# Performance work log

Hardware: AMD Instinct MI355X
Metric: run time of the kernel (lower is better)

## Reference

```python
import jax, jax.numpy as jnp
import numpy as np

LB = 8      # luma bins
CM = 1      # channel multiplier
GC = 16     # guide complexity
NIN, NOUT = 4, 3
BN_EPS = 1e-5


def bilateral_slice(grid, guide):
    # grid: [B, gh, gw, gd, C]; guide: [B, H, W] in [0,1]
    B, gh, gw, gd, C = grid.shape
    _, H, W = guide.shape
    dt = guide.dtype
    hg = (jnp.arange(H, dtype=dt) + 0.5) * (gh / H) - 0.5   # [H]
    wg = (jnp.arange(W, dtype=dt) + 0.5) * (gw / W) - 0.5   # [W]
    zg = guide * gd - 0.5                                    # [B,H,W]
    h0 = jnp.floor(hg); w0 = jnp.floor(wg); z0 = jnp.floor(zg)
    fh = hg - h0; fw = wg - w0; fz = zg - z0
    h0 = h0.astype(jnp.int32); w0 = w0.astype(jnp.int32); z0 = z0.astype(jnp.int32)
    bidx = jnp.arange(B)[:, None, None]
    out = jnp.zeros((B, H, W, C), dtype=grid.dtype)
    for dh in (0, 1):
        hi = jnp.clip(h0 + dh, 0, gh - 1)          # [H]
        wh_h = fh if dh else (1.0 - fh)
        for dw in (0, 1):
            wi = jnp.clip(w0 + dw, 0, gw - 1)      # [W]
            wh_w = fw if dw else (1.0 - fw)
            w_hw = (wh_h[:, None] * wh_w[None, :])[None]  # [1,H,W]
            for dz in (0, 1):
                zi = jnp.clip(z0 + dz, 0, gd - 1)  # [B,H,W]
                wh_z = fz if dz else (1.0 - fz)
                g = grid[bidx, hi[None, :, None], wi[None, None, :], zi]  # [B,H,W,C]
                out = out + g * (w_hw * wh_z)[..., None]
    return out


def conv1x1(x, w, b):
    # x: [B,Cin,H,W], w: [Cout,Cin], b: [Cout]
    return jnp.einsum('oc,bchw->bohw', w, x) + b[None, :, None, None]


def setup_inputs() -> dict:
    key = jax.random.key(0)
    ks = jax.random.split(key, 12)
    B, H, W, GH, GW = 4, 1024, 1024, 16, 16
    fullres = jax.random.uniform(ks[0], (B, 3, H, W), dtype=jnp.float32)
    local_features = jax.random.normal(ks[1], (B, 8 * CM * LB, GH, GW), dtype=jnp.float32)
    global_features = jax.random.normal(ks[2], (B, 8 * CM * LB), dtype=jnp.float32)
    cout = LB * NOUT * NIN  # 96
    fusion_w = jax.random.normal(ks[3], (cout, 8 * CM * LB), dtype=jnp.float32) * 0.1
    fusion_b = jnp.zeros((cout,), dtype=jnp.float32)
    g1_w = jax.random.normal(ks[4], (GC, 3), dtype=jnp.float32) * 0.5
    g1_b = jnp.zeros((GC,), dtype=jnp.float32)
    bn_gamma = jnp.ones((GC,), dtype=jnp.float32)
    bn_beta = jnp.zeros((GC,), dtype=jnp.float32)
    bn_mean = jnp.zeros((GC,), dtype=jnp.float32)
    bn_var = jnp.ones((GC,), dtype=jnp.float32)
    g2_w = jax.random.normal(ks[5], (1, GC), dtype=jnp.float32) * 0.3
    g2_b = jnp.zeros((1,), dtype=jnp.float32)
    return dict(fullres=fullres, local_features=local_features, global_features=global_features,
                fusion_w=fusion_w, fusion_b=fusion_b, g1_w=g1_w, g1_b=g1_b,
                bn_gamma=bn_gamma, bn_beta=bn_beta, bn_mean=bn_mean, bn_var=bn_var,
                g2_w=g2_w, g2_b=g2_b)


def reference(fullres, local_features, global_features, fusion_w, fusion_b,
              g1_w, g1_b, bn_gamma, bn_beta, bn_mean, bn_var, g2_w, g2_b):
    B = fullres.shape[0]
    # Fusion: relu(local + broadcast global), then 1x1 conv to 96 channels
    fused = jax.nn.relu(local_features + global_features[:, :, None, None])
    x = conv1x1(fused, fusion_w, fusion_b)                    # [B,96,GH,GW]
    GH, GW = x.shape[2], x.shape[3]
    # split(12, dim=1) + stack(dim=2) -> [B,12,LB,GH,GW]
    coeffs = x.reshape(B, LB, NIN * NOUT, GH, GW).transpose(0, 2, 1, 3, 4)
    # GuideNN: 1x1 conv + BN(eval) + relu, then 1x1 conv + sigmoid
    g = conv1x1(fullres, g1_w, g1_b)
    g = (g - bn_mean[None, :, None, None]) * (bn_gamma[None, :, None, None] *
        jax.lax.rsqrt(bn_var + BN_EPS)[None, :, None, None]) + bn_beta[None, :, None, None]
    g = jax.nn.relu(g)
    guide = jax.nn.sigmoid(conv1x1(g, g2_w, g2_b))[:, 0]      # [B,H,W]
    # Slicing: permute grid to [B,GH,GW,LB,12], trilinear slice, back to NCHW
    grid = coeffs.transpose(0, 3, 4, 2, 1)
    sliced = bilateral_slice(grid, guide)                     # [B,H,W,12]
    coeff = sliced.transpose(0, 3, 1, 2)                      # [B,12,H,W]
    # ApplyCoeffs
    R = jnp.sum(fullres * coeff[:, 0:3], axis=1, keepdims=True) + coeff[:, 9:10]
    G = jnp.sum(fullres * coeff[:, 3:6], axis=1, keepdims=True) + coeff[:, 10:11]
    Bc = jnp.sum(fullres * coeff[:, 6:9], axis=1, keepdims=True) + coeff[:, 11:12]
    return jnp.tanh(jnp.concatenate([R, G, Bc], axis=1))
```

## Files before the change

### kernel.cpp

```cpp
#include <hip/hip_runtime.h>
#include <math.h>


#define GRIDBUF_FLOATS (4 * 16 * 16 * 96)
#define CELL_STRIDE 100

typedef float  vfloat4 __attribute__((ext_vector_type(4)));
typedef float  f2      __attribute__((ext_vector_type(2)));
typedef int    i2      __attribute__((ext_vector_type(2)));

__device__ inline f2 splat2(float x) { f2 v; v.x = x; v.y = x; return v; }

__device__ inline f2 fast_tanh2(f2 x) {
    f2 ax = __builtin_elementwise_abs(x);
    f2 xx = ax + ax;
    f2 e;
    e.x = __expf(xx.x);
    e.y = __expf(xx.y);
    f2 ep1 = e + splat2(1.0f);
    f2 r;
    r.x = __builtin_amdgcn_rcpf(ep1.x);
    r.y = __builtin_amdgcn_rcpf(ep1.y);
    f2 t = splat2(1.0f) - (r + r);
    i2 sgn = __builtin_bit_cast(i2, x) & (i2){(int)0x80000000, (int)0x80000000};
    return __builtin_bit_cast(f2, __builtin_bit_cast(i2, t) | sgn);
}

__global__ __launch_bounds__(128) void coeff_kernel(
    const float* __restrict__ lf,
    const float* __restrict__ gf,
    const float* __restrict__ fw,
    const float* __restrict__ fb,
    const float* __restrict__ g1w,
    const float* __restrict__ g1b,
    const float* __restrict__ bng,
    const float* __restrict__ bnb,
    const float* __restrict__ bnm,
    const float* __restrict__ bnv,
    const float* __restrict__ g2w,
    const float* __restrict__ g2b,
    float* __restrict__ gridbuf,
    float* __restrict__ params)
{
    __shared__ float fused[64];
    const int blk = blockIdx.x;
    const int b   = blk >> 8;
    const int pos = blk & 255;
    const int t   = threadIdx.x;

    if (t < 64) {
        float v = lf[(b * 64 + t) * 256 + pos] + gf[b * 64 + t];
        fused[t] = v > 0.0f ? v : 0.0f;
    }
    __syncthreads();

    if (t < 96) {
        float acc = fb[t];
        const float* wrow = fw + t * 64;
#pragma unroll
        for (int i = 0; i < 64; ++i) acc = fmaf(wrow[i], fused[i], acc);
        gridbuf[blk * 96 + t] = acc;
    }

    if (blk == 0 && t >= 96 && t < 112) {
        int k = t - 96;
        float a = bng[k] * rsqrtf(bnv[k] + 1e-5f);
        params[k]      = g1w[k * 3 + 0] * a;
        params[16 + k] = g1w[k * 3 + 1] * a;
        params[32 + k] = g1w[k * 3 + 2] * a;
        params[48 + k] = (g1b[k] - bnm[k]) * a + bnb[k];
        params[64 + k] = g2w[k];
        if (k == 0) params[80] = g2b[0];
    }
}

__global__ __launch_bounds__(256) void slice_apply_kernel(
    const float* __restrict__ fullres,
    const float* __restrict__ gridbuf,
    const float* __restrict__ params,
    float* __restrict__ out)
{
    __shared__ __align__(16) float hrow[16 * CELL_STRIDE];

    const int t    = threadIdx.x;
    const int blk  = blockIdx.x;
    const int b    = blk >> 11;
    const int rem  = blk & 2047;
    const int y    = rem >> 1;
    const int half = rem & 1;
    const int x0   = half << 9;

    const int xb      = x0 + (t << 1);
    const int pixbase = (y << 10) + xb;
    const int planeB  = (b * 3) << 20;

    f2 rr = *(const f2*)(fullres + planeB + (0 << 20) + pixbase);
    f2 gg = *(const f2*)(fullres + planeB + (1 << 20) + pixbase);
    f2 bb = *(const f2*)(fullres + planeB + (2 << 20) + pixbase);

    {
        const int h0i  = (y < 32) ? -1 : ((y - 32) >> 6);
        const float fh = ((float)y * 0.015625f + (0.0078125f - 0.5f)) - (float)h0i;
        const int hc0  = h0i < 0 ? 0 : h0i;
        const int hc1  = (h0i + 1) > 15 ? 15 : (h0i + 1);
        const float* row0 = gridbuf + (b * 256 + hc0 * 16) * 96;
        const float* row1 = gridbuf + (b * 256 + hc1 * 16) * 96;
        const float wfh0 = 1.0f - fh;
        const int cbase = half * 7;
        if (t < 216) {
            const int i   = cbase * 96 + (t << 2);
            const int wc  = i / 96;
            const int rm  = i - wc * 96;
            float4 a = *(const float4*)(row0 + i);
            float4 c = *(const float4*)(row1 + i);
            float4 r;
            r.x = fmaf(wfh0, a.x, fh * c.x);
            r.y = fmaf(wfh0, a.y, fh * c.y);
            r.z = fmaf(wfh0, a.z, fh * c.z);
            r.w = fmaf(wfh0, a.w, fh * c.w);
            *(float4*)(hrow + wc * CELL_STRIDE + rm) = r;
        }
    }
    __syncthreads();

    const int w0i = (xb < 32) ? -1 : ((xb - 32) >> 6);
    const int wc0 = w0i < 0 ? 0 : w0i;
    const int wc1 = (w0i + 1) > 15 ? 15 : (w0i + 1);
    const float fw0 = (float)xb * 0.015625f + (0.0078125f - 0.5f) - (float)w0i;
    const float* cell0 = hrow + wc0 * CELL_STRIDE;
    const float* cell1 = hrow + wc1 * CELL_STRIDE;

    f2 acc = splat2(params[80]);
#pragma unroll
    for (int k = 0; k < 16; ++k) {
        f2 gk = __builtin_elementwise_fma(rr, splat2(params[k]),
                __builtin_elementwise_fma(gg, splat2(params[16 + k]),
                __builtin_elementwise_fma(bb, splat2(params[32 + k]),
                                          splat2(params[48 + k]))));
        gk = __builtin_elementwise_max(gk, splat2(0.0f));
        acc = __builtin_elementwise_fma(gk, splat2(params[64 + k]), acc);
    }
    f2 zg;
    zg.x = fmaf(8.0f, __builtin_amdgcn_rcpf(1.0f + __expf(-acc.x)), -0.5f);
    zg.y = fmaf(8.0f, __builtin_amdgcn_rcpf(1.0f + __expf(-acc.y)), -0.5f);

    f2 Rp, Gp, Bp;
#pragma unroll
    for (int px = 0; px < 2; ++px) {
        const float zgp = px ? zg.y : zg.x;
        int   z0 = (int)floorf(zgp);
        float fz = zgp - (float)z0;
        int zc0 = z0 < 0 ? 0 : z0;
        int zc1 = (z0 + 1) > 7 ? 7 : (z0 + 1);

        const float fw_ = fw0 + (float)px * 0.015625f;
        const float ww0 = 1.0f - fw_;
        const f2 W00 = splat2(ww0 * (1.0f - fz));
        const f2 W01 = splat2(ww0 * fz);
        const f2 W10 = splat2(fw_ * (1.0f - fz));
        const f2 W11 = splat2(fw_ * fz);

        const float4* p00 = (const float4*)(cell0 + zc0 * 12);
        const float4* p01 = (const float4*)(cell0 + zc1 * 12);
        const float4* p10 = (const float4*)(cell1 + zc0 * 12);
        const float4* p11 = (const float4*)(cell1 + zc1 * 12);

        f2 sa[6];
#pragma unroll
        for (int q = 0; q < 3; ++q) {
            float4 a = p00[q], c = p01[q], d = p10[q], e = p11[q];
            f2 alo = (f2){a.x, a.y}, ahi = (f2){a.z, a.w};
            f2 clo = (f2){c.x, c.y}, chi = (f2){c.z, c.w};
            f2 dlo = (f2){d.x, d.y}, dhi = (f2){d.z, d.w};
            f2 elo = (f2){e.x, e.y}, ehi = (f2){e.z, e.w};
            sa[2 * q] =
                __builtin_elementwise_fma(alo, W00,
                __builtin_elementwise_fma(clo, W01,
                __builtin_elementwise_fma(dlo, W10, elo * W11)));
            sa[2 * q + 1] =
                __builtin_elementwise_fma(ahi, W00,
                __builtin_elementwise_fma(chi, W01,
                __builtin_elementwise_fma(dhi, W10, ehi * W11)));
        }

        const float rs = px ? rr.y : rr.x;
        const float gs = px ? gg.y : gg.x;
        const float bs = px ? bb.y : bb.x;
        float Rv = fmaf(rs, sa[0].x, fmaf(gs, sa[0].y, fmaf(bs, sa[1].x, sa[4].y)));
        float Gv = fmaf(rs, sa[1].y, fmaf(gs, sa[2].x, fmaf(bs, sa[2].y, sa[5].x)));
        float Bv = fmaf(rs, sa[3].x, fmaf(gs, sa[3].y, fmaf(bs, sa[4].x, sa[5].y)));
        if (px == 0) { Rp.x = Rv; Gp.x = Gv; Bp.x = Bv; }
        else         { Rp.y = Rv; Gp.y = Gv; Bp.y = Bv; }
    }

    f2 tR = fast_tanh2(Rp);
    f2 tG = fast_tanh2(Gp);
    f2 tB = fast_tanh2(Bp);

    __builtin_nontemporal_store(tR, (f2*)(out + planeB + (0 << 20) + pixbase));
    __builtin_nontemporal_store(tG, (f2*)(out + planeB + (1 << 20) + pixbase));
    __builtin_nontemporal_store(tB, (f2*)(out + planeB + (2 << 20) + pixbase));
}

extern "C" void kernel_launch(void* const* d_in, const int* in_sizes, int n_in,
                              void* d_out, int out_size, void* d_ws, size_t ws_size,
                              hipStream_t stream) {
    const float* fullres = (const float*)d_in[0];
    const float* lf      = (const float*)d_in[1];
    const float* gf      = (const float*)d_in[2];
    const float* fw      = (const float*)d_in[3];
    const float* fb      = (const float*)d_in[4];
    const float* g1w     = (const float*)d_in[5];
    const float* g1b     = (const float*)d_in[6];
    const float* bng     = (const float*)d_in[7];
    const float* bnb     = (const float*)d_in[8];
    const float* bnm     = (const float*)d_in[9];
    const float* bnv     = (const float*)d_in[10];
    const float* g2w     = (const float*)d_in[11];
    const float* g2b     = (const float*)d_in[12];
    float* out = (float*)d_out;

    float* gridbuf = (float*)d_ws;
    float* params  = gridbuf + GRIDBUF_FLOATS;

    coeff_kernel<<<4 * 256, 128, 0, stream>>>(lf, gf, fw, fb, g1w, g1b,
                                              bng, bnb, bnm, bnv, g2w, g2b,
                                              gridbuf, params);
    slice_apply_kernel<<<4 * 2048, 256, 0, stream>>>(fullres, gridbuf, params, out);
}
```

Before: 129.9 us.

## Loop over batch inside slice kernel with double-buffered LDS and prefetch

Each block now handles one row-half for all four batch images instead of one. It double-buffers the shared grid row and prefetches the next image's pixels and grid rows while computing the current one. This amortizes per-block setup (index math, coordinate computation) and overlaps global loads with compute. In exchange there are 4x fewer blocks (2048), which lowers occupancy and parallelism, and register pressure rises from the prefetched values.

```diff
diff --git a/kernel.cpp b/kernel.cpp
--- a/kernel.cpp
+++ b/kernel.cpp
@@ -5,9 +5,8 @@
 #define GRIDBUF_FLOATS (4 * 16 * 16 * 96)
 #define CELL_STRIDE 100
 
-typedef float  vfloat4 __attribute__((ext_vector_type(4)));
-typedef float  f2      __attribute__((ext_vector_type(2)));
-typedef int    i2      __attribute__((ext_vector_type(2)));
+typedef float  f2  __attribute__((ext_vector_type(2)));
+typedef int    i2  __attribute__((ext_vector_type(2)));
 
 __device__ inline f2 splat2(float x) { f2 v; v.x = x; v.y = x; return v; }
 
@@ -80,126 +79,147 @@
     const float* __restrict__ params,
     float* __restrict__ out)
 {
-    __shared__ __align__(16) float hrow[16 * CELL_STRIDE];
+    __shared__ __align__(16) float hbuf[2][16 * CELL_STRIDE];
 
     const int t    = threadIdx.x;
-    const int blk  = blockIdx.x;
-    const int b    = blk >> 11;
-    const int rem  = blk & 2047;
-    const int y    = rem >> 1;
-    const int half = rem & 1;
-    const int x0   = half << 9;
-
-    const int xb      = x0 + (t << 1);
+    const int i    = blockIdx.x;
+    const int y    = i >> 1;
+    const int half = i & 1;
+    const int xb   = (half << 9) + (t << 1);
     const int pixbase = (y << 10) + xb;
-    const int planeB  = (b * 3) << 20;
-
-    f2 rr = *(const f2*)(fullres + planeB + (0 << 20) + pixbase);
-    f2 gg = *(const f2*)(fullres + planeB + (1 << 20) + pixbase);
-    f2 bb = *(const f2*)(fullres + planeB + (2 << 20) + pixbase);
-
-    {
-        const int h0i  = (y < 32) ? -1 : ((y - 32) >> 6);
-        const float fh = ((float)y * 0.015625f + (0.0078125f - 0.5f)) - (float)h0i;
-        const int hc0  = h0i < 0 ? 0 : h0i;
-        const int hc1  = (h0i + 1) > 15 ? 15 : (h0i + 1);
-        const float* row0 = gridbuf + (b * 256 + hc0 * 16) * 96;
-        const float* row1 = gridbuf + (b * 256 + hc1 * 16) * 96;
-        const float wfh0 = 1.0f - fh;
-        const int cbase = half * 7;
-        if (t < 216) {
-            const int i   = cbase * 96 + (t << 2);
-            const int wc  = i / 96;
-            const int rm  = i - wc * 96;
-            float4 a = *(const float4*)(row0 + i);
-            float4 c = *(const float4*)(row1 + i);
-            float4 r;
-            r.x = fmaf(wfh0, a.x, fh * c.x);
-            r.y = fmaf(wfh0, a.y, fh * c.y);
-            r.z = fmaf(wfh0, a.z, fh * c.z);
-            r.w = fmaf(wfh0, a.w, fh * c.w);
-            *(float4*)(hrow + wc * CELL_STRIDE + rm) = r;
-        }
-    }
-    __syncthreads();
+
+    const int h0i  = (y < 32) ? -1 : ((y - 32) >> 6);
+    const float fh = ((float)y * 0.015625f + (0.0078125f - 0.5f)) - (float)h0i;
+    const int hc0  = h0i < 0 ? 0 : h0i;
+    const int hc1  = (h0i + 1) > 15 ? 15 : (h0i + 1);
+    const float wfh0 = 1.0f - fh;
+
+    const int cbase = half * 7;
+    const int fi   = cbase * 96 + (t << 2);
+    const int fwc  = fi / 96;
+    const int frm  = fi - fwc * 96;
+    const int fill_off = fwc * CELL_STRIDE + frm;
+    const float* grow0 = gridbuf + hc0 * 16 * 96 + fi;
+    const float* grow1 = gridbuf + hc1 * 16 * 96 + fi;
 
     const int w0i = (xb < 32) ? -1 : ((xb - 32) >> 6);
     const int wc0 = w0i < 0 ? 0 : w0i;
     const int wc1 = (w0i + 1) > 15 ? 15 : (w0i + 1);
     const float fw0 = (float)xb * 0.015625f + (0.0078125f - 0.5f) - (float)w0i;
-    const float* cell0 = hrow + wc0 * CELL_STRIDE;
-    const float* cell1 = hrow + wc1 * CELL_STRIDE;
-
-    f2 acc = splat2(params[80]);
-#pragma unroll
-    for (int k = 0; k < 16; ++k) {
-        f2 gk = __builtin_elementwise_fma(rr, splat2(params[k]),
-                __builtin_elementwise_fma(gg, splat2(params[16 + k]),
-                __builtin_elementwise_fma(bb, splat2(params[32 + k]),
-                                          splat2(params[48 + k]))));
-        gk = __builtin_elementwise_max(gk, splat2(0.0f));
-        acc = __builtin_elementwise_fma(gk, splat2(params[64 + k]), acc);
-    }
-    f2 zg;
-    zg.x = fmaf(8.0f, __builtin_amdgcn_rcpf(1.0f + __expf(-acc.x)), -0.5f);
-    zg.y = fmaf(8.0f, __builtin_amdgcn_rcpf(1.0f + __expf(-acc.y)), -0.5f);
-
-    f2 Rp, Gp, Bp;
-#pragma unroll
-    for (int px = 0; px < 2; ++px) {
-        const float zgp = px ? zg.y : zg.x;
-        int   z0 = (int)floorf(zgp);
-        float fz = zgp - (float)z0;
-        int zc0 = z0 < 0 ? 0 : z0;
-        int zc1 = (z0 + 1) > 7 ? 7 : (z0 + 1);
-
-        const float fw_ = fw0 + (float)px * 0.015625f;
-        const float ww0 = 1.0f - fw_;
-        const f2 W00 = splat2(ww0 * (1.0f - fz));
-        const f2 W01 = splat2(ww0 * fz);
-        const f2 W10 = splat2(fw_ * (1.0f - fz));
-        const f2 W11 = splat2(fw_ * fz);
-
-        const float4* p00 = (const float4*)(cell0 + zc0 * 12);
-        const float4* p01 = (const float4*)(cell0 + zc1 * 12);
-        const float4* p10 = (const float4*)(cell1 + zc0 * 12);
-        const float4* p11 = (const float4*)(cell1 + zc1 * 12);
-
-        f2 sa[6];
-#pragma unroll
-        for (int q = 0; q < 3; ++q) {
-            float4 a = p00[q], c = p01[q], d = p10[q], e = p11[q];
-            f2 alo = (f2){a.x, a.y}, ahi = (f2){a.z, a.w};
-            f2 clo = (f2){c.x, c.y}, chi = (f2){c.z, c.w};
-            f2 dlo = (f2){d.x, d.y}, dhi = (f2){d.z, d.w};
-            f2 elo = (f2){e.x, e.y}, ehi = (f2){e.z, e.w};
-            sa[2 * q] =
-                __builtin_elementwise_fma(alo, W00,
-                __builtin_elementwise_fma(clo, W01,
-                __builtin_elementwise_fma(dlo, W10, elo * W11)));
-            sa[2 * q + 1] =
-                __builtin_elementwise_fma(ahi, W00,
-                __builtin_elementwise_fma(chi, W01,
-                __builtin_elementwise_fma(dhi, W10, ehi * W11)));
-        }
-
-        const float rs = px ? rr.y : rr.x;
-        const float gs = px ? gg.y : gg.x;
-        const float bs = px ? bb.y : bb.x;
-        float Rv = fmaf(rs, sa[0].x, fmaf(gs, sa[0].y, fmaf(bs, sa[1].x, sa[4].y)));
-        float Gv = fmaf(rs, sa[1].y, fmaf(gs, sa[2].x, fmaf(bs, sa[2].y, sa[5].x)));
-        float Bv = fmaf(rs, sa[3].x, fmaf(gs, sa[3].y, fmaf(bs, sa[4].x, sa[5].y)));
-        if (px == 0) { Rp.x = Rv; Gp.x = Gv; Bp.x = Bv; }
-        else         { Rp.y = Rv; Gp.y = Gv; Bp.y = Bv; }
-    }
-
-    f2 tR = fast_tanh2(Rp);
-    f2 tG = fast_tanh2(Gp);
-    f2 tB = fast_tanh2(Bp);
-
-    __builtin_nontemporal_store(tR, (f2*)(out + planeB + (0 << 20) + pixbase));
-    __builtin_nontemporal_store(tG, (f2*)(out + planeB + (1 << 20) + pixbase));
-    __builtin_nontemporal_store(tB, (f2*)(out + planeB + (2 << 20) + pixbase));
+
+    float4 ga, gc;
+    if (t < 216) {
+        ga = *(const float4*)grow0;
+        gc = *(const float4*)grow1;
+    }
+    f2 rr = *(const f2*)(fullres + pixbase);
+    f2 gg = *(const f2*)(fullres + (1 << 20) + pixbase);
+    f2 bb = *(const f2*)(fullres + (2 << 20) + pixbase);
+
+#pragma unroll
+    for (int it = 0; it < 4; ++it) {
+        float* buf = hbuf[it & 1];
+
+        if (t < 216) {
+            float4 r;
+            r.x = fmaf(wfh0, ga.x, fh * gc.x);
+            r.y = fmaf(wfh0, ga.y, fh * gc.y);
+            r.z = fmaf(wfh0, ga.z, fh * gc.z);
+            r.w = fmaf(wfh0, ga.w, fh * gc.w);
+            *(float4*)(buf + fill_off) = r;
+        }
+
+        f2 nrr, ngg, nbb;
+        float4 nga, ngc;
+        if (it < 3) {
+            const float* fr = fullres + (((it + 1) * 3) << 20) + pixbase;
+            nrr = *(const f2*)fr;
+            ngg = *(const f2*)(fr + (1 << 20));
+            nbb = *(const f2*)(fr + (2 << 20));
+            if (t < 216) {
+                nga = *(const float4*)(grow0 + (it + 1) * 24576);
+                ngc = *(const float4*)(grow1 + (it + 1) * 24576);
+            }
+        }
+        __syncthreads();
+
+        const float* cell0 = buf + wc0 * CELL_STRIDE;
+        const float* cell1 = buf + wc1 * CELL_STRIDE;
+
+        f2 acc = splat2(params[80]);
+#pragma unroll
+        for (int k = 0; k < 16; ++k) {
+            f2 gk = __builtin_elementwise_fma(rr, splat2(params[k]),
+                    __builtin_elementwise_fma(gg, splat2(params[16 + k]),
+                    __builtin_elementwise_fma(bb, splat2(params[32 + k]),
+                                              splat2(params[48 + k]))));
+            gk = __builtin_elementwise_max(gk, splat2(0.0f));
+            acc = __builtin_elementwise_fma(gk, splat2(params[64 + k]), acc);
+        }
+        f2 zg;
+        zg.x = fmaf(8.0f, __builtin_amdgcn_rcpf(1.0f + __expf(-acc.x)), -0.5f);
+        zg.y = fmaf(8.0f, __builtin_amdgcn_rcpf(1.0f + __expf(-acc.y)), -0.5f);
+
+        f2 Rp, Gp, Bp;
+#pragma unroll
+        for (int px = 0; px < 2; ++px) {
+            const float zgp = px ? zg.y : zg.x;
+            int   z0 = (int)floorf(zgp);
+            float fz = zgp - (float)z0;
+            int zc0 = z0 < 0 ? 0 : z0;
+            int zc1 = (z0 + 1) > 7 ? 7 : (z0 + 1);
+
+            const float fw_ = fw0 + (float)px * 0.015625f;
+            const float ww0 = 1.0f - fw_;
+            const f2 W00 = splat2(ww0 * (1.0f - fz));
+            const f2 W01 = splat2(ww0 * fz);
+            const f2 W10 = splat2(fw_ * (1.0f - fz));
+            const f2 W11 = splat2(fw_ * fz);
+
+            const float4* p00 = (const float4*)(cell0 + zc0 * 12);
+            const float4* p01 = (const float4*)(cell0 + zc1 * 12);
+            const float4* p10 = (const float4*)(cell1 + zc0 * 12);
+            const float4* p11 = (const float4*)(cell1 + zc1 * 12);
+
+            f2 sa[6];
+#pragma unroll
+            for (int q = 0; q < 3; ++q) {
+                float4 a = p00[q], c = p01[q], d = p10[q], e = p11[q];
+                f2 alo = (f2){a.x, a.y}, ahi = (f2){a.z, a.w};
+                f2 clo = (f2){c.x, c.y}, chi = (f2){c.z, c.w};
+                f2 dlo = (f2){d.x, d.y}, dhi = (f2){d.z, d.w};
+                f2 elo = (f2){e.x, e.y}, ehi = (f2){e.z, e.w};
+                sa[2 * q] =
+                    __builtin_elementwise_fma(alo, W00,
+                    __builtin_elementwise_fma(clo, W01,
+                    __builtin_elementwise_fma(dlo, W10, elo * W11)));
+                sa[2 * q + 1] =
+                    __builtin_elementwise_fma(ahi, W00,
+                    __builtin_elementwise_fma(chi, W01,
+                    __builtin_elementwise_fma(dhi, W10, ehi * W11)));
+            }
+
+            const float rs = px ? rr.y : rr.x;
+            const float gs = px ? gg.y : gg.x;
+            const float bs = px ? bb.y : bb.x;
+            float Rv = fmaf(rs, sa[0].x, fmaf(gs, sa[0].y, fmaf(bs, sa[1].x, sa[4].y)));
+            float Gv = fmaf(rs, sa[1].y, fmaf(gs, sa[2].x, fmaf(bs, sa[2].y, sa[5].x)));
+            float Bv = fmaf(rs, sa[3].x, fmaf(gs, sa[3].y, fmaf(bs, sa[4].x, sa[5].y)));
+            if (px == 0) { Rp.x = Rv; Gp.x = Gv; Bp.x = Bv; }
+            else         { Rp.y = Rv; Gp.y = Gv; Bp.y = Bv; }
+        }
+
+        f2 tR = fast_tanh2(Rp);
+        f2 tG = fast_tanh2(Gp);
+        f2 tB = fast_tanh2(Bp);
+
+        float* ob = out + ((it * 3) << 20) + pixbase;
+        __builtin_nontemporal_store(tR, (f2*)(ob));
+        __builtin_nontemporal_store(tG, (f2*)(ob + (1 << 20)));
+        __builtin_nontemporal_store(tB, (f2*)(ob + (2 << 20)));
+
+        ga = nga; gc = ngc; rr = nrr; gg = ngg; bb = nbb;
+    }
 }
 
 extern "C" void kernel_launch(void* const* d_in, const int* in_sizes, int n_in,
@@ -226,5 +246,5 @@
     coeff_kernel<<<4 * 256, 128, 0, stream>>>(lf, gf, fw, fb, g1w, g1b,
                                               bng, bnb, bnm, bnv, g2w, g2b,
                                               gridbuf, params);
-    slice_apply_kernel<<<4 * 2048, 256, 0, stream>>>(fullres, gridbuf, params, out);
-}
+    slice_apply_kernel<<<2048, 256, 0, stream>>>(fullres, gridbuf, params, out);
+}
```

New measurement: 132.3 us. Within noise of the previous version (+1.9%).
